# Kernel tuning notes

Hardware: AMD Instinct MI355X
Metric: run time of the kernel (lower is better)

Reference implementation:

```python
import jax, jax.numpy as jnp
import numpy as np

N = 100000   # entities
T = 4        # edge types
E = 250000   # edges per type
D = 64       # dimension
H = 4        # attention heads
C = 64       # per-head out channels (PyG out_channels)
F_IN = 256   # raw feature dim
L = 2        # num_layers
NEG_SLOPE = 0.2


def setup_inputs() -> dict:
    key = jax.random.key(0)
    ks = jax.random.split(key, 10)
    return {
        "feature_matrix": jax.random.normal(ks[0], (N, F_IN), jnp.float32),
        "entity_emb": jax.random.normal(ks[1], (N + 1, D), jnp.float32),
        "lin_w": jax.random.normal(ks[2], (F_IN, D), jnp.float32) * 0.05,
        "lin_b": jnp.zeros((D,), jnp.float32),
        "ln_g": jnp.ones((D,), jnp.float32),
        "ln_b": jnp.zeros((D,), jnp.float32),
        "W_src": jax.random.normal(ks[3], (L, T, D, H * C), jnp.float32) * 0.1,
        "W_dst": jax.random.normal(ks[4], (L, T, D, H * C), jnp.float32) * 0.1,
        "a_src": jax.random.normal(ks[5], (L, T, H, C), jnp.float32) * 0.1,
        "a_dst": jax.random.normal(ks[6], (L, T, H, C), jnp.float32) * 0.1,
        "conv_bias": jnp.zeros((L, T, C), jnp.float32),
        "edge_index": jax.random.randint(ks[7], (T, 2, E), 0, N, jnp.int32),
    }


def _layer_norm(x, g, b):
    mu = jnp.mean(x, axis=-1, keepdims=True)
    var = jnp.var(x, axis=-1, keepdims=True)
    return (x - mu) * jax.lax.rsqrt(var + 1e-5) * g + b


def _l2_normalize(x):
    n = jnp.linalg.norm(x, axis=-1, keepdims=True)
    return x / jnp.maximum(n, 1e-12)


def _gat_conv(x, src, dst, Ws, Wd, a_s, a_d, bias):
    # x: [N, D]; src/dst: [E'] (self loops already appended, PyG default)
    xs = (x @ Ws).reshape(N, H, C)          # source projection per head
    xd = (x @ Wd).reshape(N, H, C)          # destination projection per head
    logit = (xs * a_s).sum(-1)[src] + (xd * a_d).sum(-1)[dst]  # [E', H]
    logit = jax.nn.leaky_relu(logit, NEG_SLOPE)
    # segment softmax over incoming edges of each dst node
    m = jax.lax.stop_gradient(jax.ops.segment_max(logit, dst, num_segments=N))
    p = jnp.exp(logit - m[dst])
    s = jax.ops.segment_sum(p, dst, num_segments=N)
    alpha = p / s[dst]                       # [E', H]
    msg = xs[src] * alpha[..., None]         # [E', H, C]
    out = jax.ops.segment_sum(msg.reshape(-1, H * C), dst, num_segments=N)
    out = out.reshape(N, H, C).mean(axis=1)  # concat=False -> head mean
    return out + bias


def reference(feature_matrix, entity_emb, lin_w, lin_b, ln_g, ln_b,
              W_src, W_dst, a_src, a_dst, conv_bias, edge_index):
    # feature_transform: Linear -> LayerNorm -> GELU (exact erf GELU, torch default)
    xf = jax.nn.gelu(_layer_norm(feature_matrix @ lin_w + lin_b, ln_g, ln_b),
                     approximate=False)
    xe = _l2_normalize(entity_emb[:N])
    x = xf + xe
    loop = jnp.arange(N, dtype=edge_index.dtype)
    for l in range(L):
        acc = jnp.zeros((N, C), x.dtype)
        for t in range(T):
            src = jnp.concatenate([edge_index[t, 0], loop])
            dst = jnp.concatenate([edge_index[t, 1], loop])
            acc = acc + _gat_conv(x, src, dst, W_src[l, t], W_dst[l, t],
                                  a_src[l, t], a_dst[l, t], conv_bias[l, t])
        x = jax.nn.gelu(acc / T, approximate=False)  # HeteroConv aggr='mean'; dropout=eval identity
    return x
```

## Files before the change

### kernel.cpp

```cpp
#include <hip/hip_runtime.h>
#include <hip/hip_bf16.h>
#include <cstdint>

#define NN   100000
#define TT   4
#define EE   250000
#define LL   2
#define NCH  49
#define EPN  (EE + NN)
#define N64  ((size_t)NN * 64)
#define CHK  25088

typedef unsigned short ushort_t;
typedef __attribute__((ext_vector_type(8))) short bf16x8;
typedef __attribute__((ext_vector_type(16))) float floatx16;

static __device__ __forceinline__ float gelu_exact(float v) {
    return 0.5f * v * (1.0f + erff(v * 0.7071067811865476f));
}
static __device__ __forceinline__ float wave_sum64(float v) {
    #pragma unroll
    for (int m = 32; m; m >>= 1) v += __shfl_xor(v, m, 64);
    return v;
}
static __device__ __forceinline__ ushort_t f2bf(float f) {
    unsigned u = __float_as_uint(f);
    u += 0x7FFFu + ((u >> 16) & 1u);
    return (ushort_t)(u >> 16);
}
static __device__ __forceinline__ float bf2f(ushort_t h) {
    return __uint_as_float((unsigned)h << 16);
}

__global__ __launch_bounds__(256) void k_prep(
    const float* __restrict__ Wsrc, const float* __restrict__ Wdst,
    const float* __restrict__ asrc, const float* __restrict__ adst,
    const float* __restrict__ cb, const float* __restrict__ lin_w,
    ushort_t* __restrict__ wcTh, ushort_t* __restrict__ wcTl,
    ushort_t* __restrict__ lwTh, ushort_t* __restrict__ lwTl,
    ushort_t* __restrict__ bpTh, ushort_t* __restrict__ bpTl,
    float* __restrict__ bsum)
{
    int id = blockIdx.x * 256 + threadIdx.x;
    {
        int d = id & 63;
        int c = (id >> 6) & 63;
        int h = (id >> 12) & 3;
        int t = (id >> 14) & 3;
        int l = (id >> 16) & 1;
        float v = 0.25f * Wsrc[(((l * 4 + t) * 64 + d) * 256) + h * 64 + c];
        int dst = (l * 64 + c) * 1024 + (t * 256 + h * 64 + d);
        ushort_t hh = f2bf(v);
        bpTh[dst] = hh;
        bpTl[dst] = f2bf(v - bf2f(hh));
    }
    if (id < LL * 64 * 64) {
        int d   = id & 63;
        int col = (id >> 6) & 63;
        int l   = (id >> 12) & 1;
        int t = col >> 3, side = (col >> 2) & 1, h = col & 3;
        const float* W = side ? Wdst : Wsrc;
        const float* a = side ? adst : asrc;
        int wb = ((l * 4 + t) * 64 + d) * 256 + h * 64;
        int ab = ((l * 4 + t) * 4 + h) * 64;
        float s = 0.f;
        #pragma unroll 8
        for (int c2 = 0; c2 < 64; ++c2) s = fmaf(W[wb + c2], a[ab + c2], s);
        int dst = (l * 64 + col) * 64 + d;
        ushort_t hh = f2bf(s);
        wcTh[dst] = hh;
        wcTl[dst] = f2bf(s - bf2f(hh));
    }
    if (id < 64 * 256) {
        int k = id & 255, c = id >> 8;
        float v = lin_w[k * 64 + c];
        ushort_t hh = f2bf(v);
        lwTh[c * 256 + k] = hh;
        lwTl[c * 256 + k] = f2bf(v - bf2f(hh));
    }
    if (id < LL * 64) {
        int l = id >> 6, c = id & 63;
        float s = 0.f;
        for (int t = 0; t < TT; ++t) s += cb[(l * 4 + t) * 64 + c];
        bsum[id] = s;
    }
}

__global__ void k_hist(const int* __restrict__ ei, int* __restrict__ cursor) {
    int id = blockIdx.x * 256 + threadIdx.x;
    if (id >= TT * EE) return;
    int t = id / EE, e = id - t * EE;
    int d = ei[(t * 2 + 1) * EE + e];
    atomicAdd(&cursor[t * NN + d], 1);
}

__global__ __launch_bounds__(256) void k_scan1(const int* __restrict__ deg,
                                               int* __restrict__ csum) {
    int b = blockIdx.x, t = b / NCH, cc = b - t * NCH;
    int tid = threadIdx.x;
    int base = cc * 2048 + tid * 8;
    int s = 0;
    #pragma unroll
    for (int i = 0; i < 8; ++i) {
        int idx = base + i;
        if (idx < NN) s += deg[t * NN + idx] + 1;
    }
    #pragma unroll
    for (int m = 32; m; m >>= 1) s += __shfl_xor(s, m, 64);
    __shared__ int ws4[4];
    int lane = tid & 63, wid = tid >> 6;
    if (lane == 0) ws4[wid] = s;
    __syncthreads();
    if (tid == 0) csum[b] = ws4[0] + ws4[1] + ws4[2] + ws4[3];
}

__global__ void k_scan2(const int* __restrict__ csum, int* __restrict__ cbase,
                        int* __restrict__ row_ptr) {
    int t = threadIdx.x;
    if (t >= TT) return;
    int base = 0;
    for (int c = 0; c < NCH; ++c) {
        cbase[t * NCH + c] = base;
        base += csum[t * NCH + c];
    }
    row_ptr[t * (NN + 1) + NN] = base;
}

__global__ __launch_bounds__(256) void k_scan3(int* __restrict__ cursor,
                                               const int* __restrict__ cbase,
                                               int* __restrict__ row_ptr) {
    int b = blockIdx.x, t = b / NCH, cc = b - t * NCH;
    int tid = threadIdx.x, lane = tid & 63, wid = tid >> 6;
    int base = cc * 2048 + tid * 8;
    int vals[8], ts = 0;
    #pragma unroll
    for (int i = 0; i < 8; ++i) {
        int idx = base + i;
        int v = (idx < NN) ? cursor[t * NN + idx] + 1 : 0;
        vals[i] = v; ts += v;
    }
    int v = ts;
    #pragma unroll
    for (int off = 1; off < 64; off <<= 1) {
        int u = __shfl_up(v, off, 64);
        if (lane >= off) v += u;
    }
    __shared__ int wt[4];
    if (lane == 63) wt[wid] = v;
    __syncthreads();
    int wbase = 0;
    for (int w = 0; w < wid; ++w) wbase += wt[w];
    int run = cbase[t * NCH + cc] + wbase + (v - ts);
    #pragma unroll
    for (int i = 0; i < 8; ++i) {
        int idx = base + i;
        if (idx < NN) {
            row_ptr[t * (NN + 1) + idx] = run;
            cursor[t * NN + idx] = run;
        }
        run += vals[i];
    }
}

__global__ void k_scatter(const int* __restrict__ ei, int* __restrict__ cursor,
                          int* __restrict__ col, int* __restrict__ dstarr) {
    int id = blockIdx.x * 256 + threadIdx.x;
    if (id >= TT * EPN) return;
    int t = id / EPN, r = id - t * EPN;
    int s, d;
    if (r < EE) { s = ei[t * 2 * EE + r]; d = ei[(t * 2 + 1) * EE + r]; }
    else        { s = d = r - EE; }
    int pos = atomicAdd(&cursor[t * NN + d], 1);
    col[(size_t)t * EPN + pos] = s;
    dstarr[(size_t)t * EPN + pos] = d;
}

template <int FLAGS>
__global__ __launch_bounds__(256, 4) void k_gemm_mx(
    const ushort_t* __restrict__ Ahi, const ushort_t* __restrict__ Alo,
    const ushort_t* __restrict__ Bhi, const ushort_t* __restrict__ Blo,
    int K, int ldb, int nrows,
    const float* __restrict__ bias, float* __restrict__ Cout)
{
    constexpr int KC = 32, LK = 40;
    __shared__ ushort_t sAh[128 * LK], sAl[128 * LK];
    __shared__ ushort_t sBh[64 * LK],  sBl[64 * LK];
    const int tid = threadIdx.x;
    const int w = tid >> 6, ln = tid & 63;
    const int l31 = ln & 31, hl = ln >> 5;
    const int rowbase = blockIdx.x * 128;

    floatx16 accv[2];
    #pragma unroll
    for (int ct = 0; ct < 2; ++ct)
        #pragma unroll
        for (int r = 0; r < 16; ++r) accv[ct][r] = 0.f;

    for (int kc = 0; kc < K; kc += KC) {
        __syncthreads();
        #pragma unroll
        for (int i = 0; i < 2; ++i) {
            int f = tid + i * 256;
            int r = f >> 2, cg = f & 3;
            int row = rowbase + r;
            int so = r * LK + cg * 8;
            if (row < nrows) {
                size_t ga = (size_t)row * K + kc + cg * 8;
                if constexpr (FLAGS & 8) {
                    const float* Af = (const float*)Ahi;
                    float4 v0 = *(const float4*)(Af + ga);
                    float4 v1 = *(const float4*)(Af + ga + 4);
                    float vf[8] = {v0.x, v0.y, v0.z, v0.w, v1.x, v1.y, v1.z, v1.w};
                    unsigned hu[8], lu[8];
                    #pragma unroll
                    for (int q = 0; q < 8; ++q) {
                        ushort_t hh = f2bf(vf[q]);
                        hu[q] = hh;
                        lu[q] = f2bf(vf[q] - bf2f(hh));
                    }
                    uint4 H = make_uint4(hu[0] | (hu[1] << 16), hu[2] | (hu[3] << 16),
                                         hu[4] | (hu[5] << 16), hu[6] | (hu[7] << 16));
                    uint4 L = make_uint4(lu[0] | (lu[1] << 16), lu[2] | (lu[3] << 16),
                                         lu[4] | (lu[5] << 16), lu[6] | (lu[7] << 16));
                    *(uint4*)&sAh[so] = H;
                    *(uint4*)&sAl[so] = L;
                } else {
                    *(uint4*)&sAh[so] = *(const uint4*)(Ahi + ga);
                    *(uint4*)&sAl[so] = *(const uint4*)(Alo + ga);
                }
            } else {
                *(uint4*)&sAh[so] = make_uint4(0, 0, 0, 0);
                *(uint4*)&sAl[so] = make_uint4(0, 0, 0, 0);
            }
        }
        {
            int r = tid >> 2, cg = tid & 3;
            size_t gb = (size_t)r * ldb + kc + cg * 8;
            int so = r * LK + cg * 8;
            *(uint4*)&sBh[so] = *(const uint4*)(Bhi + gb);
            *(uint4*)&sBl[so] = *(const uint4*)(Blo + gb);
        }
        __syncthreads();
        const int arow = (w << 5) + l31;
        #pragma unroll
        for (int s = 0; s < 2; ++s) {
            const int koff = (s << 4) + (hl << 3);
            bf16x8 ah  = *(const bf16x8*)&sAh[arow * LK + koff];
            bf16x8 al  = *(const bf16x8*)&sAl[arow * LK + koff];
            bf16x8 bh0 = *(const bf16x8*)&sBh[l31 * LK + koff];
            bf16x8 bl0 = *(const bf16x8*)&sBl[l31 * LK + koff];
            bf16x8 bh1 = *(const bf16x8*)&sBh[(32 + l31) * LK + koff];
            bf16x8 bl1 = *(const bf16x8*)&sBl[(32 + l31) * LK + koff];
            accv[0] = __builtin_amdgcn_mfma_f32_32x32x16_bf16(ah, bh0, accv[0], 0, 0, 0);
            accv[1] = __builtin_amdgcn_mfma_f32_32x32x16_bf16(ah, bh1, accv[1], 0, 0, 0);
            accv[0] = __builtin_amdgcn_mfma_f32_32x32x16_bf16(al, bh0, accv[0], 0, 0, 0);
            accv[1] = __builtin_amdgcn_mfma_f32_32x32x16_bf16(al, bh1, accv[1], 0, 0, 0);
            accv[0] = __builtin_amdgcn_mfma_f32_32x32x16_bf16(ah, bl0, accv[0], 0, 0, 0);
            accv[1] = __builtin_amdgcn_mfma_f32_32x32x16_bf16(ah, bl1, accv[1], 0, 0, 0);
        }
    }
    #pragma unroll
    for (int ct = 0; ct < 2; ++ct) {
        int col = (ct << 5) + l31;
        float bv = (FLAGS & 2) ? bias[col] : 0.f;
        #pragma unroll
        for (int r = 0; r < 16; ++r) {
            int row = rowbase + (w << 5) + (r & 3) + ((r >> 2) << 3) + (hl << 2);
            if (row < nrows) {
                size_t idx = (size_t)row * 64 + col;
                float v = accv[ct][r];
                if (FLAGS & 2) v = gelu_exact((v + bv) * 0.25f);
                Cout[idx] = v;
            }
        }
    }
}

__global__ __launch_bounds__(256) void k_feat_post(
    const float* __restrict__ y, const float* __restrict__ lin_b,
    const float* __restrict__ ln_g, const float* __restrict__ ln_b,
    const float* __restrict__ emb, float* __restrict__ xout)
{
    int n = (blockIdx.x << 2) + (threadIdx.x >> 6);
    int c = threadIdx.x & 63;
    size_t base = (size_t)n * 64 + c;
    float v = y[base] + lin_b[c];
    float mean = wave_sum64(v) * 0.015625f;
    float t = v - mean;
    float var = wave_sum64(t * t) * 0.015625f;
    float vn = t * (1.0f / sqrtf(var + 1e-5f)) * ln_g[c] + ln_b[c];
    float g = gelu_exact(vn);
    float e = emb[base];
    float nrm = sqrtf(wave_sum64(e * e));
    float xv = g + e / fmaxf(nrm, 1e-12f);
    xout[base] = xv;
}

__global__ __launch_bounds__(256) void k_edgep(
    const float* __restrict__ s_all, const int* __restrict__ col,
    const int* __restrict__ dstarr, float* __restrict__ parr)
{
    int i = blockIdx.x * 256 + threadIdx.x;
    int t = blockIdx.y;
    if (i >= EPN) return;
    size_t base = (size_t)t * EPN + i;
    int s = col[base], d = dstarr[base];
    const float4 a = *(const float4*)&s_all[(size_t)s * 64 + t * 8];
    const float4 b = *(const float4*)&s_all[(size_t)d * 64 + t * 8 + 4];
    float l0 = a.x + b.x, l1 = a.y + b.y;
    float l2 = a.z + b.z, l3 = a.w + b.w;
    l0 = l0 > 0.f ? l0 : 0.2f * l0;
    l1 = l1 > 0.f ? l1 : 0.2f * l1;
    l2 = l2 > 0.f ? l2 : 0.2f * l2;
    l3 = l3 > 0.f ? l3 : 0.2f * l3;
    float4 p = make_float4(__expf(l0), __expf(l1), __expf(l2), __expf(l3));
    *(float4*)&parr[base * 4] = p;
}

__global__ __launch_bounds__(256) void k_edge2(
    const float* __restrict__ x, const float* __restrict__ parr,
    const int* __restrict__ row_ptr, const int* __restrict__ col,
    ushort_t* __restrict__ zh, ushort_t* __restrict__ zl, int n0, int n1)
{
    int n = n0 + (blockIdx.x << 2) + (threadIdx.x >> 6);
    int lane = threadIdx.x & 63;
    if (n >= n1) return;
    #pragma unroll
    for (int t = 0; t < TT; ++t) {
        int rp0 = row_ptr[t * (NN + 1) + n];
        int rp1 = row_ptr[t * (NN + 1) + n + 1];
        const int* colt = col + (size_t)t * EPN;
        const float4* pt = (const float4*)parr + (size_t)t * EPN;
        float z0 = 0.f, z1 = 0.f, z2 = 0.f, z3 = 0.f;
        float S0 = 0.f, S1 = 0.f, S2 = 0.f, S3 = 0.f;
        #pragma unroll 2
        for (int e = rp0; e < rp1; ++e) {
            int s = colt[e];
            float4 p = pt[e];
            float xv = x[(size_t)s * 64 + lane];
            S0 += p.x; S1 += p.y; S2 += p.z; S3 += p.w;
            z0 = fmaf(p.x, xv, z0);
            z1 = fmaf(p.y, xv, z1);
            z2 = fmaf(p.z, xv, z2);
            z3 = fmaf(p.w, xv, z3);
        }
        size_t zb = (size_t)(n - n0) * 1024 + t * 256 + lane;
        float v0 = z0 / S0, v1 = z1 / S1, v2 = z2 / S2, v3 = z3 / S3;
        ushort_t h0 = f2bf(v0), h1 = f2bf(v1), h2 = f2bf(v2), h3 = f2bf(v3);
        zh[zb]       = h0;  zl[zb]       = f2bf(v0 - bf2f(h0));
        zh[zb + 64]  = h1;  zl[zb + 64]  = f2bf(v1 - bf2f(h1));
        zh[zb + 128] = h2;  zl[zb + 128] = f2bf(v2 - bf2f(h2));
        zh[zb + 192] = h3;  zl[zb + 192] = f2bf(v3 - bf2f(h3));
    }
}

extern "C" void kernel_launch(void* const* d_in, const int* in_sizes, int n_in,
                              void* d_out, int out_size, void* d_ws, size_t ws_size,
                              hipStream_t stream) {
    const float* fm    = (const float*)d_in[0];
    const float* emb   = (const float*)d_in[1];
    const float* lin_w = (const float*)d_in[2];
    const float* lin_b = (const float*)d_in[3];
    const float* ln_g  = (const float*)d_in[4];
    const float* ln_b  = (const float*)d_in[5];
    const float* Wsrc  = (const float*)d_in[6];
    const float* Wdst  = (const float*)d_in[7];
    const float* asrc  = (const float*)d_in[8];
    const float* adst  = (const float*)d_in[9];
    const float* cbias = (const float*)d_in[10];
    const int*   ei    = (const int*)d_in[11];
    float* out = (float*)d_out;
    (void)in_sizes; (void)n_in; (void)out_size;

    char* w = (char*)d_ws;
    size_t off = 0;
    auto alloc = [&](size_t bytes) -> void* {
        void* p = w + off;
        off += (bytes + 255) & ~(size_t)255;
        return p;
    };
    ushort_t* wcTh = (ushort_t*)alloc((size_t)LL * 64 * 64 * 2);
    ushort_t* wcTl = (ushort_t*)alloc((size_t)LL * 64 * 64 * 2);
    ushort_t* lwTh = (ushort_t*)alloc((size_t)64 * 256 * 2);
    ushort_t* lwTl = (ushort_t*)alloc((size_t)64 * 256 * 2);
    ushort_t* bpTh = (ushort_t*)alloc((size_t)LL * 64 * 1024 * 2);
    ushort_t* bpTl = (ushort_t*)alloc((size_t)LL * 64 * 1024 * 2);
    float* bsum    = (float*)alloc((size_t)LL * 64 * 4);
    int*   row_ptr = (int*)  alloc((size_t)TT * (NN + 1) * 4);
    int*   cursor  = (int*)  alloc((size_t)TT * NN * 4);
    int*   colarr  = (int*)  alloc((size_t)TT * EPN * 4);
    int*   dstarr  = (int*)  alloc((size_t)TT * EPN * 4);
    float* parr    = (float*)alloc((size_t)TT * EPN * 4 * 4);
    int*   csum    = (int*)  alloc((size_t)TT * NCH * 4);
    int*   cbase   = (int*)  alloc((size_t)TT * NCH * 4);
    float* x       = (float*)alloc(N64 * 4);
    float* xnew    = (float*)alloc(N64 * 4);
    float* s_all   = (float*)alloc(N64 * 4);
    float* ybuf    = (float*)alloc(N64 * 4);
    size_t planeE = (size_t)CHK * 1024;
    ushort_t* zh = (ushort_t*)alloc(2 * planeE * 2);
    ushort_t* zl = zh + planeE;

    hipMemsetAsync(cursor, 0, (size_t)TT * NN * 4, stream);
    k_prep<<<512, 256, 0, stream>>>(Wsrc, Wdst, asrc, adst, cbias, lin_w,
                                    wcTh, wcTl, lwTh, lwTl, bpTh, bpTl, bsum);
    k_hist<<<(TT * EE + 255) / 256, 256, 0, stream>>>(ei, cursor);
    k_scan1<<<TT * NCH, 256, 0, stream>>>(cursor, csum);
    k_scan2<<<1, 64, 0, stream>>>(csum, cbase, row_ptr);
    k_scan3<<<TT * NCH, 256, 0, stream>>>(cursor, cbase, row_ptr);
    k_scatter<<<(TT * EPN + 255) / 256, 256, 0, stream>>>(ei, cursor, colarr, dstarr);

    const int GB = (NN + 127) / 128;
    k_gemm_mx<8><<<GB, 256, 0, stream>>>((const ushort_t*)fm, nullptr,
                                         lwTh, lwTl, 256, 256, NN,
                                         nullptr, ybuf);
    k_feat_post<<<NN / 4, 256, 0, stream>>>(ybuf, lin_b, ln_g, ln_b, emb, x);

    const dim3 gp((EPN + 255) / 256, TT);
    for (int l = 0; l < LL; ++l) {
        const float* xin = (l == 0) ? x : xnew;
        float* dest = (l == 0) ? xnew : out;
        k_gemm_mx<8><<<GB, 256, 0, stream>>>((const ushort_t*)xin, nullptr,
                                             wcTh + l * 4096, wcTl + l * 4096,
                                             64, 64, NN, nullptr, s_all);
        k_edgep<<<gp, 256, 0, stream>>>(s_all, colarr, dstarr, parr);
        const ushort_t* Bh = bpTh + (size_t)l * 65536;
        const ushort_t* Bl = bpTl + (size_t)l * 65536;
        for (int n0 = 0; n0 < NN; n0 += CHK) {
            int n1 = (n0 + CHK < NN) ? n0 + CHK : NN;
            int nr = n1 - n0;
            k_edge2<<<(nr + 3) / 4, 256, 0, stream>>>(xin, parr, row_ptr, colarr,
                                                      zh, zl, n0, n1);
            k_gemm_mx<2><<<(nr + 127) / 128, 256, 0, stream>>>(
                zh, zl, Bh, Bl, 1024, 1024, nr, bsum + l * 64, dest + (size_t)n0 * 64);
        }
    }
}
```

Measured before the change: 1.117 ms.

## Split edge aggregation by type pairs, swizzle LDS with direct loads, pack edges

The edge-aggregation kernel now handles two edge types per pass over all nodes, instead of four types per node chunk. The message GEMM is split into two K=512 halves: the first writes a partial result and the second adds it in the epilogue before bias and GELU. GEMM tiles are now loaded straight from global memory into LDS with global_load_lds, using an XOR swizzle instead of padding, and source/destination indices are packed into one int2 array. The aim is fewer launches, cheaper tile staging and fewer index loads, at the cost of a larger z workspace and more passes over the edge lists.

New measurement: 1.024 ms. 8.4% less time.

```diff
diff --git a/kernel.cpp b/kernel.cpp
--- a/kernel.cpp
+++ b/kernel.cpp
@@ -9,7 +9,6 @@
 #define NCH  49
 #define EPN  (EE + NN)
 #define N64  ((size_t)NN * 64)
-#define CHK  25088
 
 typedef unsigned short ushort_t;
 typedef __attribute__((ext_vector_type(8))) short bf16x8;
@@ -30,6 +29,11 @@
 }
 static __device__ __forceinline__ float bf2f(ushort_t h) {
     return __uint_as_float((unsigned)h << 16);
+}
+static __device__ __forceinline__ void gl_lds16(const ushort_t* g, ushort_t* l) {
+    __builtin_amdgcn_global_load_lds(
+        (const __attribute__((address_space(1))) void*)g,
+        (__attribute__((address_space(3))) void*)l, 16, 0, 0);
 }
 
 __global__ __launch_bounds__(256) void k_prep(
@@ -163,7 +167,7 @@
 }
 
 __global__ void k_scatter(const int* __restrict__ ei, int* __restrict__ cursor,
-                          int* __restrict__ col, int* __restrict__ dstarr) {
+                          int2* __restrict__ sd) {
     int id = blockIdx.x * 256 + threadIdx.x;
     if (id >= TT * EPN) return;
     int t = id / EPN, r = id - t * EPN;
@@ -171,8 +175,7 @@
     if (r < EE) { s = ei[t * 2 * EE + r]; d = ei[(t * 2 + 1) * EE + r]; }
     else        { s = d = r - EE; }
     int pos = atomicAdd(&cursor[t * NN + d], 1);
-    col[(size_t)t * EPN + pos] = s;
-    dstarr[(size_t)t * EPN + pos] = d;
+    sd[(size_t)t * EPN + pos] = make_int2(s, d);
 }
 
 template <int FLAGS>
@@ -180,11 +183,12 @@
     const ushort_t* __restrict__ Ahi, const ushort_t* __restrict__ Alo,
     const ushort_t* __restrict__ Bhi, const ushort_t* __restrict__ Blo,
     int K, int ldb, int nrows,
-    const float* __restrict__ bias, float* __restrict__ Cout)
+    const float* __restrict__ accbuf, const float* __restrict__ bias,
+    float* __restrict__ Cout)
 {
-    constexpr int KC = 32, LK = 40;
-    __shared__ ushort_t sAh[128 * LK], sAl[128 * LK];
-    __shared__ ushort_t sBh[64 * LK],  sBl[64 * LK];
+    constexpr int KC = 32;
+    __shared__ ushort_t sAh[128 * 32], sAl[128 * 32];
+    __shared__ ushort_t sBh[64 * 32],  sBl[64 * 32];
     const int tid = threadIdx.x;
     const int w = tid >> 6, ln = tid & 63;
     const int l31 = ln & 31, hl = ln >> 5;
@@ -203,11 +207,12 @@
             int f = tid + i * 256;
             int r = f >> 2, cg = f & 3;
             int row = rowbase + r;
-            int so = r * LK + cg * 8;
-            if (row < nrows) {
-                size_t ga = (size_t)row * K + kc + cg * 8;
-                if constexpr (FLAGS & 8) {
+            int sg = (r ^ (r >> 2)) & 3;
+            if constexpr (FLAGS & 8) {
+                int sw = r * 32 + ((cg ^ sg) << 3);
+                if (row < nrows) {
                     const float* Af = (const float*)Ahi;
+                    size_t ga = (size_t)row * K + kc + cg * 8;
                     float4 v0 = *(const float4*)(Af + ga);
                     float4 v1 = *(const float4*)(Af + ga + 4);
                     float vf[8] = {v0.x, v0.y, v0.z, v0.w, v1.x, v1.y, v1.z, v1.w};
@@ -222,35 +227,44 @@
                                          hu[4] | (hu[5] << 16), hu[6] | (hu[7] << 16));
                     uint4 L = make_uint4(lu[0] | (lu[1] << 16), lu[2] | (lu[3] << 16),
                                          lu[4] | (lu[5] << 16), lu[6] | (lu[7] << 16));
-                    *(uint4*)&sAh[so] = H;
-                    *(uint4*)&sAl[so] = L;
+                    *(uint4*)&sAh[sw] = H;
+                    *(uint4*)&sAl[sw] = L;
                 } else {
-                    *(uint4*)&sAh[so] = *(const uint4*)(Ahi + ga);
-                    *(uint4*)&sAl[so] = *(const uint4*)(Alo + ga);
+                    *(uint4*)&sAh[sw] = make_uint4(0, 0, 0, 0);
+                    *(uint4*)&sAl[sw] = make_uint4(0, 0, 0, 0);
                 }
             } else {
-                *(uint4*)&sAh[so] = make_uint4(0, 0, 0, 0);
-                *(uint4*)&sAl[so] = make_uint4(0, 0, 0, 0);
+                int so = r * 32 + (cg << 3);
+                size_t ga = (size_t)row * K + kc + ((cg ^ sg) << 3);
+                if (row < nrows) {
+                    gl_lds16(Ahi + ga, &sAh[so]);
+                    gl_lds16(Alo + ga, &sAl[so]);
+                }
             }
         }
         {
             int r = tid >> 2, cg = tid & 3;
-            size_t gb = (size_t)r * ldb + kc + cg * 8;
-            int so = r * LK + cg * 8;
-            *(uint4*)&sBh[so] = *(const uint4*)(Bhi + gb);
-            *(uint4*)&sBl[so] = *(const uint4*)(Blo + gb);
+            int sg = (r ^ (r >> 2)) & 3;
+            int so = r * 32 + (cg << 3);
+            size_t gb = (size_t)r * ldb + kc + ((cg ^ sg) << 3);
+            gl_lds16(Bhi + gb, &sBh[so]);
+            gl_lds16(Blo + gb, &sBl[so]);
         }
         __syncthreads();
         const int arow = (w << 5) + l31;
+        const int sga = (arow ^ (arow >> 2)) & 3;
+        const int sgb = (l31 ^ (l31 >> 2)) & 3;
         #pragma unroll
         for (int s = 0; s < 2; ++s) {
-            const int koff = (s << 4) + (hl << 3);
-            bf16x8 ah  = *(const bf16x8*)&sAh[arow * LK + koff];
-            bf16x8 al  = *(const bf16x8*)&sAl[arow * LK + koff];
-            bf16x8 bh0 = *(const bf16x8*)&sBh[l31 * LK + koff];
-            bf16x8 bl0 = *(const bf16x8*)&sBl[l31 * LK + koff];
-            bf16x8 bh1 = *(const bf16x8*)&sBh[(32 + l31) * LK + koff];
-            bf16x8 bl1 = *(const bf16x8*)&sBl[(32 + l31) * LK + koff];
+            const int c0 = (s << 1) | hl;
+            const int ka = (c0 ^ sga) << 3;
+            const int kb = (c0 ^ sgb) << 3;
+            bf16x8 ah  = *(const bf16x8*)&sAh[arow * 32 + ka];
+            bf16x8 al  = *(const bf16x8*)&sAl[arow * 32 + ka];
+            bf16x8 bh0 = *(const bf16x8*)&sBh[l31 * 32 + kb];
+            bf16x8 bl0 = *(const bf16x8*)&sBl[l31 * 32 + kb];
+            bf16x8 bh1 = *(const bf16x8*)&sBh[(32 + l31) * 32 + kb];
+            bf16x8 bl1 = *(const bf16x8*)&sBl[(32 + l31) * 32 + kb];
             accv[0] = __builtin_amdgcn_mfma_f32_32x32x16_bf16(ah, bh0, accv[0], 0, 0, 0);
             accv[1] = __builtin_amdgcn_mfma_f32_32x32x16_bf16(ah, bh1, accv[1], 0, 0, 0);
             accv[0] = __builtin_amdgcn_mfma_f32_32x32x16_bf16(al, bh0, accv[0], 0, 0, 0);
@@ -269,6 +283,7 @@
             if (row < nrows) {
                 size_t idx = (size_t)row * 64 + col;
                 float v = accv[ct][r];
+                if (FLAGS & 1) v += accbuf[idx];
                 if (FLAGS & 2) v = gelu_exact((v + bv) * 0.25f);
                 Cout[idx] = v;
             }
@@ -297,16 +312,16 @@
 }
 
 __global__ __launch_bounds__(256) void k_edgep(
-    const float* __restrict__ s_all, const int* __restrict__ col,
-    const int* __restrict__ dstarr, float* __restrict__ parr)
+    const float* __restrict__ s_all, const int2* __restrict__ sd,
+    float* __restrict__ parr)
 {
     int i = blockIdx.x * 256 + threadIdx.x;
     int t = blockIdx.y;
     if (i >= EPN) return;
     size_t base = (size_t)t * EPN + i;
-    int s = col[base], d = dstarr[base];
-    const float4 a = *(const float4*)&s_all[(size_t)s * 64 + t * 8];
-    const float4 b = *(const float4*)&s_all[(size_t)d * 64 + t * 8 + 4];
+    int2 e = sd[base];
+    const float4 a = *(const float4*)&s_all[(size_t)e.x * 64 + t * 8];
+    const float4 b = *(const float4*)&s_all[(size_t)e.y * 64 + t * 8 + 4];
     float l0 = a.x + b.x, l1 = a.y + b.y;
     float l2 = a.z + b.z, l3 = a.w + b.w;
     l0 = l0 > 0.f ? l0 : 0.2f * l0;
@@ -319,38 +334,72 @@
 
 __global__ __launch_bounds__(256) void k_edge2(
     const float* __restrict__ x, const float* __restrict__ parr,
-    const int* __restrict__ row_ptr, const int* __restrict__ col,
-    ushort_t* __restrict__ zh, ushort_t* __restrict__ zl, int n0, int n1)
+    const int* __restrict__ row_ptr, const int2* __restrict__ sd,
+    ushort_t* __restrict__ zh, ushort_t* __restrict__ zl, int t0)
 {
-    int n = n0 + (blockIdx.x << 2) + (threadIdx.x >> 6);
+    int n = (blockIdx.x << 2) + (threadIdx.x >> 6);
     int lane = threadIdx.x & 63;
-    if (n >= n1) return;
-    #pragma unroll
-    for (int t = 0; t < TT; ++t) {
-        int rp0 = row_ptr[t * (NN + 1) + n];
-        int rp1 = row_ptr[t * (NN + 1) + n + 1];
-        const int* colt = col + (size_t)t * EPN;
-        const float4* pt = (const float4*)parr + (size_t)t * EPN;
-        float z0 = 0.f, z1 = 0.f, z2 = 0.f, z3 = 0.f;
-        float S0 = 0.f, S1 = 0.f, S2 = 0.f, S3 = 0.f;
-        #pragma unroll 2
-        for (int e = rp0; e < rp1; ++e) {
-            int s = colt[e];
-            float4 p = pt[e];
-            float xv = x[(size_t)s * 64 + lane];
-            S0 += p.x; S1 += p.y; S2 += p.z; S3 += p.w;
-            z0 = fmaf(p.x, xv, z0);
-            z1 = fmaf(p.y, xv, z1);
-            z2 = fmaf(p.z, xv, z2);
-            z3 = fmaf(p.w, xv, z3);
-        }
-        size_t zb = (size_t)(n - n0) * 1024 + t * 256 + lane;
-        float v0 = z0 / S0, v1 = z1 / S1, v2 = z2 / S2, v3 = z3 / S3;
+    const int tA = t0, tB = t0 + 1;
+    int eA  = row_ptr[tA * (NN + 1) + n];
+    int eA1 = row_ptr[tA * (NN + 1) + n + 1];
+    int eB  = row_ptr[tB * (NN + 1) + n];
+    int eB1 = row_ptr[tB * (NN + 1) + n + 1];
+    const int2*   sdA = sd + (size_t)tA * EPN;
+    const float4* pA  = (const float4*)parr + (size_t)tA * EPN;
+    const int2*   sdB = sd + (size_t)tB * EPN;
+    const float4* pB  = (const float4*)parr + (size_t)tB * EPN;
+    float a0 = 0.f, a1 = 0.f, a2 = 0.f, a3 = 0.f;
+    float SA0 = 0.f, SA1 = 0.f, SA2 = 0.f, SA3 = 0.f;
+    float b0 = 0.f, b1 = 0.f, b2 = 0.f, b3 = 0.f;
+    float SB0 = 0.f, SB1 = 0.f, SB2 = 0.f, SB3 = 0.f;
+    int m = (eA1 - eA < eB1 - eB) ? (eA1 - eA) : (eB1 - eB);
+    #pragma unroll 2
+    for (int i = 0; i < m; ++i) {
+        int sA_ = sdA[eA + i].x;
+        int sB_ = sdB[eB + i].x;
+        float4 pa = pA[eA + i];
+        float4 pb = pB[eB + i];
+        float xa = x[(size_t)sA_ * 64 + lane];
+        float xb = x[(size_t)sB_ * 64 + lane];
+        SA0 += pa.x; SA1 += pa.y; SA2 += pa.z; SA3 += pa.w;
+        SB0 += pb.x; SB1 += pb.y; SB2 += pb.z; SB3 += pb.w;
+        a0 = fmaf(pa.x, xa, a0); a1 = fmaf(pa.y, xa, a1);
+        a2 = fmaf(pa.z, xa, a2); a3 = fmaf(pa.w, xa, a3);
+        b0 = fmaf(pb.x, xb, b0); b1 = fmaf(pb.y, xb, b1);
+        b2 = fmaf(pb.z, xb, b2); b3 = fmaf(pb.w, xb, b3);
+    }
+    eA += m; eB += m;
+    for (; eA < eA1; ++eA) {
+        int s = sdA[eA].x; float4 p = pA[eA];
+        float xv = x[(size_t)s * 64 + lane];
+        SA0 += p.x; SA1 += p.y; SA2 += p.z; SA3 += p.w;
+        a0 = fmaf(p.x, xv, a0); a1 = fmaf(p.y, xv, a1);
+        a2 = fmaf(p.z, xv, a2); a3 = fmaf(p.w, xv, a3);
+    }
+    for (; eB < eB1; ++eB) {
+        int s = sdB[eB].x; float4 p = pB[eB];
+        float xv = x[(size_t)s * 64 + lane];
+        SB0 += p.x; SB1 += p.y; SB2 += p.z; SB3 += p.w;
+        b0 = fmaf(p.x, xv, b0); b1 = fmaf(p.y, xv, b1);
+        b2 = fmaf(p.z, xv, b2); b3 = fmaf(p.w, xv, b3);
+    }
+    size_t zb = (size_t)n * 512 + lane;
+    {
+        float v0 = a0 / SA0, v1 = a1 / SA1, v2 = a2 / SA2, v3 = a3 / SA3;
         ushort_t h0 = f2bf(v0), h1 = f2bf(v1), h2 = f2bf(v2), h3 = f2bf(v3);
         zh[zb]       = h0;  zl[zb]       = f2bf(v0 - bf2f(h0));
         zh[zb + 64]  = h1;  zl[zb + 64]  = f2bf(v1 - bf2f(h1));
         zh[zb + 128] = h2;  zl[zb + 128] = f2bf(v2 - bf2f(h2));
         zh[zb + 192] = h3;  zl[zb + 192] = f2bf(v3 - bf2f(h3));
+    }
+    {
+        size_t zc = zb + 256;
+        float v0 = b0 / SB0, v1 = b1 / SB1, v2 = b2 / SB2, v3 = b3 / SB3;
+        ushort_t h0 = f2bf(v0), h1 = f2bf(v1), h2 = f2bf(v2), h3 = f2bf(v3);
+        zh[zc]       = h0;  zl[zc]       = f2bf(v0 - bf2f(h0));
+        zh[zc + 64]  = h1;  zl[zc + 64]  = f2bf(v1 - bf2f(h1));
+        zh[zc + 128] = h2;  zl[zc + 128] = f2bf(v2 - bf2f(h2));
+        zh[zc + 192] = h3;  zl[zc + 192] = f2bf(v3 - bf2f(h3));
     }
 }
 
@@ -370,7 +419,7 @@
     const float* cbias = (const float*)d_in[10];
     const int*   ei    = (const int*)d_in[11];
     float* out = (float*)d_out;
-    (void)in_sizes; (void)n_in; (void)out_size;
+    (void)in_sizes; (void)n_in; (void)out_size; (void)ws_size;
 
     char* w = (char*)d_ws;
     size_t off = 0;
@@ -388,16 +437,14 @@
     float* bsum    = (float*)alloc((size_t)LL * 64 * 4);
     int*   row_ptr = (int*)  alloc((size_t)TT * (NN + 1) * 4);
     int*   cursor  = (int*)  alloc((size_t)TT * NN * 4);
-    int*   colarr  = (int*)  alloc((size_t)TT * EPN * 4);
-    int*   dstarr  = (int*)  alloc((size_t)TT * EPN * 4);
+    int2*  sdarr   = (int2*) alloc((size_t)TT * EPN * 8);
     float* parr    = (float*)alloc((size_t)TT * EPN * 4 * 4);
     int*   csum    = (int*)  alloc((size_t)TT * NCH * 4);
     int*   cbase   = (int*)  alloc((size_t)TT * NCH * 4);
     float* x       = (float*)alloc(N64 * 4);
-    float* xnew    = (float*)alloc(N64 * 4);
     float* s_all   = (float*)alloc(N64 * 4);
-    float* ybuf    = (float*)alloc(N64 * 4);
-    size_t planeE = (size_t)CHK * 1024;
+    float* accB    = (float*)alloc(N64 * 4);
+    size_t planeE = (size_t)NN * 512;
     ushort_t* zh = (ushort_t*)alloc(2 * planeE * 2);
     ushort_t* zl = zh + planeE;
 
@@ -408,31 +455,28 @@
     k_scan1<<<TT * NCH, 256, 0, stream>>>(cursor, csum);
     k_scan2<<<1, 64, 0, stream>>>(csum, cbase, row_ptr);
     k_scan3<<<TT * NCH, 256, 0, stream>>>(cursor, cbase, row_ptr);
-    k_scatter<<<(TT * EPN + 255) / 256, 256, 0, stream>>>(ei, cursor, colarr, dstarr);
+    k_scatter<<<(TT * EPN + 255) / 256, 256, 0, stream>>>(ei, cursor, sdarr);
 
     const int GB = (NN + 127) / 128;
     k_gemm_mx<8><<<GB, 256, 0, stream>>>((const ushort_t*)fm, nullptr,
                                          lwTh, lwTl, 256, 256, NN,
-                                         nullptr, ybuf);
-    k_feat_post<<<NN / 4, 256, 0, stream>>>(ybuf, lin_b, ln_g, ln_b, emb, x);
+                                         nullptr, nullptr, accB);
+    k_feat_post<<<NN / 4, 256, 0, stream>>>(accB, lin_b, ln_g, ln_b, emb, x);
 
     const dim3 gp((EPN + 255) / 256, TT);
     for (int l = 0; l < LL; ++l) {
-        const float* xin = (l == 0) ? x : xnew;
-        float* dest = (l == 0) ? xnew : out;
-        k_gemm_mx<8><<<GB, 256, 0, stream>>>((const ushort_t*)xin, nullptr,
+        float* dest = (l == 0) ? x : out;
+        k_gemm_mx<8><<<GB, 256, 0, stream>>>((const ushort_t*)x, nullptr,
                                              wcTh + l * 4096, wcTl + l * 4096,
-                                             64, 64, NN, nullptr, s_all);
-        k_edgep<<<gp, 256, 0, stream>>>(s_all, colarr, dstarr, parr);
+                                             64, 64, NN, nullptr, nullptr, s_all);
+        k_edgep<<<gp, 256, 0, stream>>>(s_all, sdarr, parr);
         const ushort_t* Bh = bpTh + (size_t)l * 65536;
         const ushort_t* Bl = bpTl + (size_t)l * 65536;
-        for (int n0 = 0; n0 < NN; n0 += CHK) {
-            int n1 = (n0 + CHK < NN) ? n0 + CHK : NN;
-            int nr = n1 - n0;
-            k_edge2<<<(nr + 3) / 4, 256, 0, stream>>>(xin, parr, row_ptr, colarr,
-                                                      zh, zl, n0, n1);
-            k_gemm_mx<2><<<(nr + 127) / 128, 256, 0, stream>>>(
-                zh, zl, Bh, Bl, 1024, 1024, nr, bsum + l * 64, dest + (size_t)n0 * 64);
-        }
-    }
-}
+        k_edge2<<<NN / 4, 256, 0, stream>>>(x, parr, row_ptr, sdarr, zh, zl, 0);
+        k_gemm_mx<0><<<GB, 256, 0, stream>>>(zh, zl, Bh, Bl, 512, 1024, NN,
+                                             nullptr, nullptr, accB);
+        k_edge2<<<NN / 4, 256, 0, stream>>>(x, parr, row_ptr, sdarr, zh, zl, 2);
+        k_gemm_mx<3><<<GB, 256, 0, stream>>>(zh, zl, Bh + 512, Bl + 512, 512, 1024,
+                                             NN, accB, bsum + l * 64, dest);
+    }
+}
```
